# Optimization experiments

Measured on AMD Instinct MI355X. Metric: run time of the kernel, lower is better.

Reference implementation:

```python
import jax, jax.numpy as jnp
import numpy as np

B, T, IN, H = 32, 1024, 1024, 512
L = 2          # num_layers
D = 2          # num_directions (bidirectional)
P_IN, P_H = 0.33, 0.33


def setup_inputs() -> dict:
    key = jax.random.key(0)
    ks = jax.random.split(key, 8)
    stdv = 1.0 / np.sqrt(H)  # default_initializer: uniform(-stdv, stdv)
    x = jax.random.normal(ks[0], (B, T, IN), jnp.float32)
    # sequence mask (1 = valid token, 0 = pad)
    mask = (jax.random.uniform(ks[1], (B, T)) < 0.95).astype(jnp.float32)
    w_ih = jax.random.uniform(ks[2], (L * D, H, IN), jnp.float32, -stdv, stdv)
    w_hh = jax.random.uniform(ks[3], (L * D, H, H), jnp.float32, -stdv, stdv)
    b_ih = jnp.zeros((L * D, H), jnp.float32)  # 1-D params init to 0
    b_hh = jnp.zeros((L * D, H), jnp.float32)
    # variational dropout: one Bernoulli mask per cell, shared across time
    noise_in = (jax.random.bernoulli(ks[4], 1.0 - P_IN, (L * D, B, IN))
                .astype(jnp.float32) / (1.0 - P_IN))
    noise_h = (jax.random.bernoulli(ks[5], 1.0 - P_H, (L * D, B, H))
               .astype(jnp.float32) / (1.0 - P_H))
    return {"x": x, "mask": mask, "w_ih": w_ih, "w_hh": w_hh,
            "b_ih": b_ih, "b_hh": b_hh, "noise_in": noise_in, "noise_h": noise_h}


def _rnn_forward(x, mask, w_ih, w_hh, b_ih, b_hh, noise_in, noise_h):
    xt = jnp.transpose(x, (1, 0, 2))          # [T,B,IN] (batch_first input)
    m = jnp.transpose(mask)[:, :, None]       # [T,B,1]

    def run_dir(seq_in, c, reverse):
        # precompute input projection: W_ih @ (x * noise_in) + b_ih, all steps
        xin = jnp.einsum('tbi,hi->tbh', seq_in * noise_in[c][None], w_ih[c]) + b_ih[c]
        whh_t = w_hh[c].T
        nh = noise_h[c]
        bh = b_hh[c]

        def step(h, inp):
            xb, mt = inp
            h_new = jnp.tanh(xb + (h * nh) @ whh_t + bh)
            h = h_new * mt + h * (1.0 - mt)   # mask gating
            return h, h

        h0 = jnp.zeros((B, H), seq_in.dtype)
        h_last, hs = jax.lax.scan(step, h0, (xin, m), reverse=reverse)
        return hs, h_last                      # hs: [T,B,H] in original time order

    seq = xt
    finals = []
    for layer in range(L):
        hf, ff = run_dir(seq, layer * D + 0, False)
        hb, fb = run_dir(seq, layer * D + 1, True)
        seq = jnp.concatenate([hf, hb], axis=-1)  # [T,B,2H]
        finals.append(ff)
        finals.append(fb)

    output = jnp.transpose(seq, (1, 0, 2))    # [B,T,2H] (batch_first)
    hn = jnp.stack(finals, axis=0)            # [L*D,B,H]
    return output, hn


def reference(x, mask, w_ih, w_hh, b_ih, b_hh, noise_in, noise_h):
    return _rnn_forward(x, mask, w_ih, w_hh, b_ih, b_hh, noise_in, noise_h)
```

## Files before the change

### kernel.cpp

```cpp
#include <hip/hip_runtime.h>
#include <math.h>


#define BB 32
#define TT 1024
#define HH 512
#define KK 1024

typedef _Float16 f16x8 __attribute__((ext_vector_type(8)));
typedef float f32x4 __attribute__((ext_vector_type(4)));

__global__ __launch_bounds__(256)
void proj_kernel(const float* __restrict__ src, const float* __restrict__ noise,
                 const float* __restrict__ wih, const float* __restrict__ bih,
                 float* __restrict__ dst, int src_tmajor)
{
    __shared__ float As[16][68];
    __shared__ float Bs[16][132];

    const int tid = threadIdx.x;
    const int bm = blockIdx.x & 511;
    const int bn = blockIdx.x >> 9;
    const int mbase = bm * 64;
    const int nbase = bn * 128;

    const int aRow = tid >> 2;
    const int aK   = (tid & 3) * 4;
    const int m    = mbase + aRow;
    const int t    = m >> 5;
    const int b    = m & 31;
    const size_t srcRow = (size_t)(src_tmajor ? m : (b * TT + t)) * KK;
    const float* __restrict__ nrow = noise + (size_t)b * KK;

    const int wRow = tid >> 1;
    const int wK   = (tid & 1) * 8;
    const size_t wBase = (size_t)(nbase + wRow) * KK;

    const int tm = (tid >> 4) * 4;
    const int tn = (tid & 15) * 4;

    float acc[4][8];
#pragma unroll
    for (int i = 0; i < 4; ++i)
#pragma unroll
        for (int j = 0; j < 8; ++j) acc[i][j] = 0.f;

    for (int k0 = 0; k0 < KK; k0 += 16) {
        __syncthreads();
        {
            float4 v  = *(const float4*)(src + srcRow + k0 + aK);
            float4 nz = *(const float4*)(nrow + k0 + aK);
            As[aK + 0][aRow] = v.x * nz.x;
            As[aK + 1][aRow] = v.y * nz.y;
            As[aK + 2][aRow] = v.z * nz.z;
            As[aK + 3][aRow] = v.w * nz.w;
        }
        {
            float4 v0 = *(const float4*)(wih + wBase + k0 + wK);
            float4 v1 = *(const float4*)(wih + wBase + k0 + wK + 4);
            Bs[wK + 0][wRow] = v0.x;
            Bs[wK + 1][wRow] = v0.y;
            Bs[wK + 2][wRow] = v0.z;
            Bs[wK + 3][wRow] = v0.w;
            Bs[wK + 4][wRow] = v1.x;
            Bs[wK + 5][wRow] = v1.y;
            Bs[wK + 6][wRow] = v1.z;
            Bs[wK + 7][wRow] = v1.w;
        }
        __syncthreads();
#pragma unroll
        for (int kk = 0; kk < 16; ++kk) {
            float4 a  = *(const float4*)&As[kk][tm];
            float4 bL = *(const float4*)&Bs[kk][tn];
            float4 bH = *(const float4*)&Bs[kk][tn + 64];
            float av[4] = {a.x, a.y, a.z, a.w};
            float bv[8] = {bL.x, bL.y, bL.z, bL.w, bH.x, bH.y, bH.z, bH.w};
#pragma unroll
            for (int i = 0; i < 4; ++i)
#pragma unroll
                for (int j = 0; j < 8; ++j)
                    acc[i][j] = fmaf(av[i], bv[j], acc[i][j]);
        }
    }

    float4 bL = *(const float4*)(bih + nbase + tn);
    float4 bH = *(const float4*)(bih + nbase + tn + 64);
#pragma unroll
    for (int i = 0; i < 4; ++i) {
        size_t row = (size_t)(mbase + tm + i) * HH;
        float4 o0 = {acc[i][0] + bL.x, acc[i][1] + bL.y,
                     acc[i][2] + bL.z, acc[i][3] + bL.w};
        float4 o1 = {acc[i][4] + bH.x, acc[i][5] + bH.y,
                     acc[i][6] + bH.z, acc[i][7] + bH.w};
        *(float4*)(dst + row + nbase + tn)      = o0;
        *(float4*)(dst + row + nbase + tn + 64) = o1;
    }
}

__global__ __launch_bounds__(256, 1)
void rec4_kernel(const float* __restrict__ xinF, const float* __restrict__ xinB,
                 const float* __restrict__ whh, const float* __restrict__ bhh,
                 const float* __restrict__ nh, const float* __restrict__ maskp,
                 float* __restrict__ outBase, float* __restrict__ finals,
                 unsigned long long* __restrict__ gbase,
                 unsigned* __restrict__ fbase,
                 int layer, int out_tmajor)
{
    __shared__ __align__(16) unsigned long long gsQ[2048];
    __shared__ float outs[16][272];

    const int tid   = threadIdx.x;
    const int d     = blockIdx.x & 1;
    const int grp   = (blockIdx.x >> 1) & 1;
    const int slice = (blockIdx.x >> 2) & 1;
    const int c     = layer * 2 + d;

    const int lane = tid & 63;
    const int wv   = tid >> 6;
    const int l15  = lane & 15;
    const int l4   = lane >> 4;

    const float* __restrict__ xin = d ? xinB : xinF;

    unsigned long long* exch = gbase + (size_t)((c * 2 + grp) * 2) * 2048;
    unsigned* myflag = fbase + (((c * 2 + grp) * 2 + slice) * 16);
    unsigned* pflag  = fbase + (((c * 2 + grp) * 2 + (1 - slice)) * 16);

    f16x8 Bf[4][16];
    {
        const float* wb = whh + ((size_t)c * HH + slice * 256) * HH;
#pragma unroll
        for (int j = 0; j < 4; ++j) {
            const float* wr = wb + (size_t)((wv * 4 + j) * 16 + l15) * HH + l4 * 8;
#pragma unroll
            for (int kq = 0; kq < 16; ++kq) {
                const float* p = wr + kq * 32;
                f16x8 v;
#pragma unroll
                for (int i = 0; i < 8; ++i) v[i] = (_Float16)p[i];
                Bf[j][kq] = v;
            }
        }
    }

    const int pb  = tid & 15;
    const int pn0 = (tid >> 4) * 16;
    const int gb  = grp * 16 + pb;
    float nh_r[16], bias_r[16], hold[16];
    {
        const float* np = nh + ((size_t)c * BB + gb) * HH + slice * 256 + pn0;
        const float* bp = bhh + (size_t)c * HH + slice * 256 + pn0;
#pragma unroll
        for (int i = 0; i < 16; ++i) {
            nh_r[i] = np[i]; bias_r[i] = bp[i]; hold[i] = 0.f;
        }
    }

#pragma unroll
    for (int q = 0; q < 8; ++q) gsQ[q * 256 + tid] = 0ull;

    float xr[16], mr;
    {
        const int t0 = d ? (TT - 1) : 0;
        const float* xp = xin + ((size_t)t0 * BB + gb) * HH + slice * 256 + pn0;
#pragma unroll
        for (int q = 0; q < 4; ++q) {
            float4 v = *(const float4*)(xp + q * 4);
            xr[q*4+0] = v.x + bias_r[q*4+0];
            xr[q*4+1] = v.y + bias_r[q*4+1];
            xr[q*4+2] = v.z + bias_r[q*4+2];
            xr[q*4+3] = v.w + bias_r[q*4+3];
        }
        mr = maskp[(size_t)gb * TT + t0];
    }
    __syncthreads();

    for (int s = 0; s < TT; ++s) {
        const int t = d ? (TT - 1 - s) : s;

        if (s > 0) {
            unsigned it = 0;
            while (__hip_atomic_load(pflag, __ATOMIC_RELAXED,
                                     __HIP_MEMORY_SCOPE_AGENT) < (unsigned)s) {
                __builtin_amdgcn_s_sleep(1);
                if (++it > (1u << 24)) break;
            }
            const unsigned long long* src =
                exch + (size_t)(s & 1) * 2048 + (size_t)(1 - slice) * 1024;
            unsigned long long* dst = gsQ + (size_t)(1 - slice) * 1024;
#pragma unroll
            for (int q = 0; q < 4; ++q)
                dst[q * 256 + tid] = __hip_atomic_load(&src[q * 256 + tid],
                                                       __ATOMIC_RELAXED,
                                                       __HIP_MEMORY_SCOPE_AGENT);
        }
        __syncthreads();

        f32x4 acc[4];
#pragma unroll
        for (int j = 0; j < 4; ++j) acc[j] = (f32x4){0.f, 0.f, 0.f, 0.f};
#pragma unroll
        for (int kq = 0; kq < 16; ++kq) {
            f16x8 A = *(const f16x8*)&gsQ[((size_t)(kq * 4 + l4) * 16 + l15) * 2];
#pragma unroll
            for (int j = 0; j < 4; ++j)
                acc[j] = __builtin_amdgcn_mfma_f32_16x16x32_f16(A, Bf[j][kq],
                                                                acc[j], 0, 0, 0);
        }
#pragma unroll
        for (int j = 0; j < 4; ++j) {
            const int n0 = (wv * 4 + j) * 16 + l15;
#pragma unroll
            for (int r = 0; r < 4; ++r)
                outs[l4 * 4 + r][n0] = acc[j][r];
        }
        __syncthreads();

        float hv[16];
#pragma unroll
        for (int i = 0; i < 16; ++i) {
            float pre = outs[pb][pn0 + i] + xr[i];
            float e  = exp2f(2.885390082f * pre);
            float th = 1.f - 2.f * __builtin_amdgcn_rcpf(e + 1.f);
            float hn = hold[i] + mr * (th - hold[i]);
            hold[i] = hn;
            hv[i]   = hn;
        }
        if (s + 1 < TT) {
            union Q { _Float16 h[4]; unsigned long long q; } u[4];
#pragma unroll
            for (int q = 0; q < 4; ++q)
#pragma unroll
                for (int i = 0; i < 4; ++i)
                    u[q].h[i] = (_Float16)(hv[q * 4 + i] * nh_r[q * 4 + i]);
            const int o0 = slice * 32 + (pn0 >> 3);
            unsigned long long* gl = &gsQ[((size_t)o0 * 16 + pb) * 2];
            gl[0]  = u[0].q;  gl[1]  = u[1].q;
            gl[32] = u[2].q;  gl[33] = u[3].q;
            unsigned long long* gw = exch + (size_t)((s + 1) & 1) * 2048
                                   + ((size_t)o0 * 16 + pb) * 2;
            __hip_atomic_store(&gw[0],  u[0].q, __ATOMIC_RELAXED, __HIP_MEMORY_SCOPE_AGENT);
            __hip_atomic_store(&gw[1],  u[1].q, __ATOMIC_RELAXED, __HIP_MEMORY_SCOPE_AGENT);
            __hip_atomic_store(&gw[32], u[2].q, __ATOMIC_RELAXED, __HIP_MEMORY_SCOPE_AGENT);
            __hip_atomic_store(&gw[33], u[3].q, __ATOMIC_RELAXED, __HIP_MEMORY_SCOPE_AGENT);
        }
        __syncthreads();

        if (tid == 0 && s + 1 < TT)
            __hip_atomic_store(myflag, (unsigned)(s + 1),
                               __ATOMIC_RELAXED, __HIP_MEMORY_SCOPE_AGENT);

        {
            const size_t orow = out_tmajor
                ? ((size_t)((size_t)t * BB + gb) * 1024)
                : ((size_t)((size_t)gb * TT + t) * 1024);
            float* op = outBase + orow + d * HH + slice * 256 + pn0;
#pragma unroll
            for (int q = 0; q < 4; ++q) {
                float4 v = {hv[q*4+0], hv[q*4+1], hv[q*4+2], hv[q*4+3]};
                *(float4*)(op + q * 4) = v;
            }
        }
        if (s + 1 < TT) {
            const int tn = d ? (TT - 2 - s) : (s + 1);
            const float* xp = xin + ((size_t)tn * BB + gb) * HH + slice * 256 + pn0;
#pragma unroll
            for (int q = 0; q < 4; ++q) {
                float4 v = *(const float4*)(xp + q * 4);
                xr[q*4+0] = v.x + bias_r[q*4+0];
                xr[q*4+1] = v.y + bias_r[q*4+1];
                xr[q*4+2] = v.z + bias_r[q*4+2];
                xr[q*4+3] = v.w + bias_r[q*4+3];
            }
            mr = maskp[(size_t)gb * TT + tn];
        }
    }

    {
        float* fp = finals + ((size_t)c * BB + gb) * HH + slice * 256 + pn0;
#pragma unroll
        for (int q = 0; q < 4; ++q) {
            float4 v = {hold[q*4+0], hold[q*4+1], hold[q*4+2], hold[q*4+3]};
            *(float4*)(fp + q * 4) = v;
        }
    }
}

extern "C" void kernel_launch(void* const* d_in, const int* in_sizes, int n_in,
                              void* d_out, int out_size, void* d_ws, size_t ws_size,
                              hipStream_t stream)
{
    (void)in_sizes; (void)n_in; (void)out_size; (void)ws_size;

    const float* x    = (const float*)d_in[0];
    const float* mask = (const float*)d_in[1];
    const float* wih  = (const float*)d_in[2];
    const float* whh  = (const float*)d_in[3];
    const float* bih  = (const float*)d_in[4];
    const float* bhh  = (const float*)d_in[5];
    const float* nin  = (const float*)d_in[6];
    const float* nh   = (const float*)d_in[7];

    float* out    = (float*)d_out;
    float* xinF   = (float*)d_ws;
    float* xinB   = xinF + (size_t)TT * BB * HH;
    unsigned long long* gbase =
        (unsigned long long*)(xinB + (size_t)TT * BB * HH);
    unsigned* fbase = (unsigned*)(gbase + 16 * 2048);
    float* seq0   = out;
    float* finals = out + (size_t)BB * TT * 1024;

    hipMemsetAsync(gbase, 0, 16 * 2048 * sizeof(unsigned long long) + 16 * 64,
                   stream);

    proj_kernel<<<2048, 256, 0, stream>>>(x, nin + 0 * (size_t)BB * KK,
                                          wih + 0 * (size_t)HH * KK,
                                          bih + 0 * HH, xinF, 0);
    proj_kernel<<<2048, 256, 0, stream>>>(x, nin + 1 * (size_t)BB * KK,
                                          wih + 1 * (size_t)HH * KK,
                                          bih + 1 * HH, xinB, 0);
    rec4_kernel<<<8, 256, 0, stream>>>(xinF, xinB, whh, bhh, nh, mask,
                                       seq0, finals, gbase, fbase, 0, 1);
    proj_kernel<<<2048, 256, 0, stream>>>(seq0, nin + 2 * (size_t)BB * KK,
                                          wih + 2 * (size_t)HH * KK,
                                          bih + 2 * HH, xinF, 1);
    proj_kernel<<<2048, 256, 0, stream>>>(seq0, nin + 3 * (size_t)BB * KK,
                                          wih + 3 * (size_t)HH * KK,
                                          bih + 3 * HH, xinB, 1);
    rec4_kernel<<<8, 256, 0, stream>>>(xinF, xinB, whh, bhh, nh, mask,
                                       out, finals, gbase, fbase, 1, 0);
}
```

Measured before the change: 11.66 ms.

## Replace flag-based cross-block handshake with sequence-tagged exchange words

The recurrent kernel no longer has each block publish a separate step flag after a block-wide barrier. Instead, every 32-bit half of the exchanged fp16 hidden-state data is packed into a 64-bit word whose upper half carries the step number. Consumers spin on the data itself until every word shows the expected tag. This removes one __syncthreads and the flag store/poll round trip from the serial per-step critical path. In exchange it doubles the exchange buffer size and the global traffic per step, and uses a tighter spin limit.

Result: faster. 11.18 ms (-4.1%).

```diff
diff --git a/kernel.cpp b/kernel.cpp
--- a/kernel.cpp
+++ b/kernel.cpp
@@ -98,12 +98,11 @@
 }
 
 __global__ __launch_bounds__(256, 1)
-void rec4_kernel(const float* __restrict__ xinF, const float* __restrict__ xinB,
+void rec5_kernel(const float* __restrict__ xinF, const float* __restrict__ xinB,
                  const float* __restrict__ whh, const float* __restrict__ bhh,
                  const float* __restrict__ nh, const float* __restrict__ maskp,
                  float* __restrict__ outBase, float* __restrict__ finals,
                  unsigned long long* __restrict__ gbase,
-                 unsigned* __restrict__ fbase,
                  int layer, int out_tmajor)
 {
     __shared__ __align__(16) unsigned long long gsQ[2048];
@@ -122,9 +121,7 @@
 
     const float* __restrict__ xin = d ? xinB : xinF;
 
-    unsigned long long* exch = gbase + (size_t)((c * 2 + grp) * 2) * 2048;
-    unsigned* myflag = fbase + (((c * 2 + grp) * 2 + slice) * 16);
-    unsigned* pflag  = fbase + (((c * 2 + grp) * 2 + (1 - slice)) * 16);
+    unsigned long long* exch = gbase + (size_t)(c * 2 + grp) * 8192;
 
     f16x8 Bf[4][16];
     {
@@ -173,26 +170,40 @@
         }
         mr = maskp[(size_t)gb * TT + t0];
     }
-    __syncthreads();
 
     for (int s = 0; s < TT; ++s) {
         const int t = d ? (TT - 1 - s) : s;
 
         if (s > 0) {
+            const unsigned long long* src =
+                exch + (size_t)(s & 1) * 4096 + (size_t)(1 - slice) * 2048;
+            const unsigned target = (unsigned)s;
+            unsigned long long v[8];
             unsigned it = 0;
-            while (__hip_atomic_load(pflag, __ATOMIC_RELAXED,
-                                     __HIP_MEMORY_SCOPE_AGENT) < (unsigned)s) {
-                __builtin_amdgcn_s_sleep(1);
-                if (++it > (1u << 24)) break;
-            }
-            const unsigned long long* src =
-                exch + (size_t)(s & 1) * 2048 + (size_t)(1 - slice) * 1024;
+            for (;;) {
+                bool ok = true;
+#pragma unroll
+                for (int q = 0; q < 4; ++q) {
+                    v[q*2+0] = __hip_atomic_load(&src[(size_t)(tid + q*256)*2 + 0],
+                                                 __ATOMIC_RELAXED,
+                                                 __HIP_MEMORY_SCOPE_AGENT);
+                    v[q*2+1] = __hip_atomic_load(&src[(size_t)(tid + q*256)*2 + 1],
+                                                 __ATOMIC_RELAXED,
+                                                 __HIP_MEMORY_SCOPE_AGENT);
+                }
+#pragma unroll
+                for (int i = 0; i < 8; ++i)
+                    ok &= ((unsigned)(v[i] >> 32) == target);
+                if (ok) break;
+                if (++it > (1u << 18)) break;
+            }
             unsigned long long* dst = gsQ + (size_t)(1 - slice) * 1024;
 #pragma unroll
-            for (int q = 0; q < 4; ++q)
-                dst[q * 256 + tid] = __hip_atomic_load(&src[q * 256 + tid],
-                                                       __ATOMIC_RELAXED,
-                                                       __HIP_MEMORY_SCOPE_AGENT);
+            for (int q = 0; q < 4; ++q) {
+                unsigned lo = (unsigned)v[q*2+0];
+                unsigned hi = (unsigned)v[q*2+1];
+                dst[tid + q*256] = ((unsigned long long)hi << 32) | lo;
+            }
         }
         __syncthreads();
 
@@ -227,28 +238,40 @@
             hv[i]   = hn;
         }
         if (s + 1 < TT) {
-            union Q { _Float16 h[4]; unsigned long long q; } u[4];
+            union Q { _Float16 h[4]; unsigned long long q; unsigned w[2]; } u[4];
 #pragma unroll
             for (int q = 0; q < 4; ++q)
 #pragma unroll
                 for (int i = 0; i < 4; ++i)
                     u[q].h[i] = (_Float16)(hv[q * 4 + i] * nh_r[q * 4 + i]);
-            const int o0 = slice * 32 + (pn0 >> 3);
-            unsigned long long* gl = &gsQ[((size_t)o0 * 16 + pb) * 2];
+
+            const unsigned long long seqhi =
+                ((unsigned long long)(unsigned)(s + 1)) << 32;
+            unsigned long long* gw = exch + (size_t)((s + 1) & 1) * 4096
+                                   + (size_t)slice * 2048
+                                   + (size_t)((pn0 >> 3) * 64 + pb * 4);
+            __hip_atomic_store(&gw[0],  (unsigned long long)u[0].w[0] | seqhi,
+                               __ATOMIC_RELAXED, __HIP_MEMORY_SCOPE_AGENT);
+            __hip_atomic_store(&gw[1],  (unsigned long long)u[0].w[1] | seqhi,
+                               __ATOMIC_RELAXED, __HIP_MEMORY_SCOPE_AGENT);
+            __hip_atomic_store(&gw[2],  (unsigned long long)u[1].w[0] | seqhi,
+                               __ATOMIC_RELAXED, __HIP_MEMORY_SCOPE_AGENT);
+            __hip_atomic_store(&gw[3],  (unsigned long long)u[1].w[1] | seqhi,
+                               __ATOMIC_RELAXED, __HIP_MEMORY_SCOPE_AGENT);
+            __hip_atomic_store(&gw[64], (unsigned long long)u[2].w[0] | seqhi,
+                               __ATOMIC_RELAXED, __HIP_MEMORY_SCOPE_AGENT);
+            __hip_atomic_store(&gw[65], (unsigned long long)u[2].w[1] | seqhi,
+                               __ATOMIC_RELAXED, __HIP_MEMORY_SCOPE_AGENT);
+            __hip_atomic_store(&gw[66], (unsigned long long)u[3].w[0] | seqhi,
+                               __ATOMIC_RELAXED, __HIP_MEMORY_SCOPE_AGENT);
+            __hip_atomic_store(&gw[67], (unsigned long long)u[3].w[1] | seqhi,
+                               __ATOMIC_RELAXED, __HIP_MEMORY_SCOPE_AGENT);
+
+            unsigned long long* gl =
+                &gsQ[((size_t)(slice * 32 + (pn0 >> 3)) * 16 + pb) * 2];
             gl[0]  = u[0].q;  gl[1]  = u[1].q;
             gl[32] = u[2].q;  gl[33] = u[3].q;
-            unsigned long long* gw = exch + (size_t)((s + 1) & 1) * 2048
-                                   + ((size_t)o0 * 16 + pb) * 2;
-            __hip_atomic_store(&gw[0],  u[0].q, __ATOMIC_RELAXED, __HIP_MEMORY_SCOPE_AGENT);
-            __hip_atomic_store(&gw[1],  u[1].q, __ATOMIC_RELAXED, __HIP_MEMORY_SCOPE_AGENT);
-            __hip_atomic_store(&gw[32], u[2].q, __ATOMIC_RELAXED, __HIP_MEMORY_SCOPE_AGENT);
-            __hip_atomic_store(&gw[33], u[3].q, __ATOMIC_RELAXED, __HIP_MEMORY_SCOPE_AGENT);
-        }
-        __syncthreads();
-
-        if (tid == 0 && s + 1 < TT)
-            __hip_atomic_store(myflag, (unsigned)(s + 1),
-                               __ATOMIC_RELAXED, __HIP_MEMORY_SCOPE_AGENT);
+        }
 
         {
             const size_t orow = out_tmajor
@@ -306,12 +329,10 @@
     float* xinB   = xinF + (size_t)TT * BB * HH;
     unsigned long long* gbase =
         (unsigned long long*)(xinB + (size_t)TT * BB * HH);
-    unsigned* fbase = (unsigned*)(gbase + 16 * 2048);
     float* seq0   = out;
     float* finals = out + (size_t)BB * TT * 1024;
 
-    hipMemsetAsync(gbase, 0, 16 * 2048 * sizeof(unsigned long long) + 16 * 64,
-                   stream);
+    hipMemsetAsync(gbase, 0, 8 * 8192 * sizeof(unsigned long long), stream);
 
     proj_kernel<<<2048, 256, 0, stream>>>(x, nin + 0 * (size_t)BB * KK,
                                           wih + 0 * (size_t)HH * KK,
@@ -319,14 +340,14 @@
     proj_kernel<<<2048, 256, 0, stream>>>(x, nin + 1 * (size_t)BB * KK,
                                           wih + 1 * (size_t)HH * KK,
                                           bih + 1 * HH, xinB, 0);
-    rec4_kernel<<<8, 256, 0, stream>>>(xinF, xinB, whh, bhh, nh, mask,
-                                       seq0, finals, gbase, fbase, 0, 1);
+    rec5_kernel<<<8, 256, 0, stream>>>(xinF, xinB, whh, bhh, nh, mask,
+                                       seq0, finals, gbase, 0, 1);
     proj_kernel<<<2048, 256, 0, stream>>>(seq0, nin + 2 * (size_t)BB * KK,
                                           wih + 2 * (size_t)HH * KK,
                                           bih + 2 * HH, xinF, 1);
     proj_kernel<<<2048, 256, 0, stream>>>(seq0, nin + 3 * (size_t)BB * KK,
                                           wih + 3 * (size_t)HH * KK,
                                           bih + 3 * HH, xinB, 1);
-    rec4_kernel<<<8, 256, 0, stream>>>(xinF, xinB, whh, bhh, nh, mask,
-                                       out, finals, gbase, fbase, 1, 0);
+    rec5_kernel<<<8, 256, 0, stream>>>(xinF, xinB, whh, bhh, nh, mask,
+                                       out, finals, gbase, 1, 0);
 }
```
